# Performance work log

Hardware: AMD Instinct MI355X
Metric: run time of the kernel (lower is better)

Reference implementation:

```python
import jax, jax.numpy as jnp
import numpy as np

E, D, H, W = 512, 64, 64, 64
B, L = 8, 2048
STEPS = 5
OUT_SIGMA_SCALE = 2.0


def setup_inputs() -> dict:
    key = jax.random.key(0)
    ks = jax.random.split(key, 8)
    tokens = jax.random.normal(ks[0], (B, L, E), dtype=jnp.float32)
    # positions on the HxW lattice: col 0 in [0,H), col 1 in [0,W)
    pos = jax.random.uniform(ks[1], (B, L, 2), dtype=jnp.float32)
    positions = pos * jnp.array([H, W], dtype=jnp.float32)
    # learned params (fan-in scaled init, as nn.Linear/Conv2d would give)
    W_to_field = jax.random.normal(ks[2], (D, E), dtype=jnp.float32) / np.sqrt(E)
    W_from_field = jax.random.normal(ks[3], (E, D), dtype=jnp.float32) / np.sqrt(D)
    conv1_w = jax.random.normal(ks[4], (2 * D, D, 3, 3), dtype=jnp.float32) / np.sqrt(D * 9)
    conv1_b = jnp.zeros((2 * D,), dtype=jnp.float32)
    conv2_w = jax.random.normal(ks[5], (D, 2 * D, 1, 1), dtype=jnp.float32) / np.sqrt(2 * D)
    conv2_b = jnp.zeros((D,), dtype=jnp.float32)
    log_sigma = jnp.array(np.log(4.0), dtype=jnp.float32)
    return {
        "tokens": tokens, "positions": positions,
        "W_to_field": W_to_field, "W_from_field": W_from_field,
        "conv1_w": conv1_w, "conv1_b": conv1_b,
        "conv2_w": conv2_w, "conv2_b": conv2_b,
        "log_sigma": log_sigma,
    }


def _conv2d(x, w, b, pad):
    y = jax.lax.conv_general_dilated(
        x, w, window_strides=(1, 1), padding=[(pad, pad), (pad, pad)],
        dimension_numbers=("NCHW", "OIHW", "NCHW"))
    return y + b[None, :, None, None]


def _norm_gauss(dy2, dx2, sigma):
    # (B,L,H,1)+(B,L,1,W) -> (B,L,H,W), normalized over the lattice
    g = jnp.exp(-(dy2 + dx2) / (2.0 * sigma * sigma))
    return g / (jnp.sum(g, axis=(-2, -1), keepdims=True) + 1e-6)


def reference(tokens, positions, W_to_field, W_from_field,
              conv1_w, conv1_b, conv2_w, conv2_b, log_sigma):
    sigma_in = jax.nn.softplus(log_sigma) + 1e-6
    sigma_out = sigma_in * OUT_SIGMA_SCALE

    proj = jnp.einsum("ble,de->bld", tokens, W_to_field)  # (B,L,D)

    grid_y = jnp.arange(H, dtype=jnp.float32)  # (H,)
    grid_x = jnp.arange(W, dtype=jnp.float32)  # (W,)
    dy2 = (grid_y[None, None, :, None] - positions[..., 0][..., None, None]) ** 2  # (B,L,H,1)
    dx2 = (grid_x[None, None, None, :] - positions[..., 1][..., None, None]) ** 2  # (B,L,1,W)

    weights_in = _norm_gauss(dy2, dx2, sigma_in)   # (B,L,H,W)
    field = jnp.einsum("blc,blhw->bchw", proj, weights_in)  # (B,D,H,W)

    for _ in range(STEPS):
        h = jax.nn.relu(_conv2d(field, conv1_w, conv1_b, pad=1))
        field = field + _conv2d(h, conv2_w, conv2_b, pad=0)

    weights_out = _norm_gauss(dy2, dx2, sigma_out)  # (B,L,H,W)
    sampled = jnp.einsum("bchw,blhw->blc", field, weights_out)  # (B,L,D)

    tokens_out = jnp.einsum("bld,ed->ble", sampled, W_from_field)  # (B,L,E)
    return tokens_out
```

## Files before the change

### kernel.cpp

```cpp
#include <hip/hip_runtime.h>
#include <cmath>
#include <cstddef>

#define BB 8
#define LL 2048
#define EE 512
#define DD 64
#define HH 64
#define HW 4096

typedef __attribute__((ext_vector_type(8))) short short8;
typedef __attribute__((ext_vector_type(4))) short short4v;
typedef __attribute__((ext_vector_type(4))) float f32x4;

__device__ __forceinline__ int swz(int row, int k, int ldk) {
    int g = (k >> 3) ^ (row & ((ldk >> 3) - 1));
    return row * ldk + (g << 3) + (k & 7);
}

__device__ __forceinline__ unsigned short f2bf(float f) {
    unsigned u = __builtin_bit_cast(unsigned, f);
    return (unsigned short)((u + 0x7FFFu + ((u >> 16) & 1u)) >> 16);
}
__device__ __forceinline__ short4v cvt4(float4 v) {
    short4v r;
    r[0] = (short)f2bf(v.x); r[1] = (short)f2bf(v.y);
    r[2] = (short)f2bf(v.z); r[3] = (short)f2bf(v.w);
    return r;
}
#define MFMA16(acc, a, b) acc = __builtin_amdgcn_mfma_f32_16x16x32_bf16(a, b, acc, 0, 0, 0)

__global__ __launch_bounds__(256) void k_reorder(const float* __restrict__ w1,
        const float* __restrict__ w2,
        short* __restrict__ w1b, short* __restrict__ w2b) {
    int i = blockIdx.x * 256 + threadIdx.x;
    if (i < 73728) {
        int c = i & 63, o = (i >> 6) & 127, tap = i >> 13;
        w1b[i] = (short)f2bf(w1[(size_t)o * 576 + c * 9 + tap]);
    }
    if (i < 8192) w2b[i] = (short)f2bf(w2[i]);
}

__global__ __launch_bounds__(256) void k_gauss(const float* __restrict__ pos,
        const float* __restrict__ lsig,
        float* __restrict__ gyiT, float* __restrict__ gxiT,
        float* __restrict__ gyoT, float* __restrict__ gxo) {
    __shared__ float red[4][4][64];
    __shared__ float tile[64 * 65];
    int t = threadIdx.x;
    int ll = t & 63, q = t >> 6;
    int b = blockIdx.y, lt = blockIdx.x;
    int bl = b * LL + lt * 64 + ll;
    float py = pos[(size_t)bl * 2 + 0];
    float px = pos[(size_t)bl * 2 + 1];
    float ls = lsig[0];
    float si = log1pf(expf(ls)) + 1e-6f;
    float so = si * 2.0f;
    float ai = 0.5f / (si * si), ao = 0.5f / (so * so);
    float vyi[16], vxi[16], vyo[16], vxo[16];
    float pyi = 0.f, pxi = 0.f, pyo = 0.f, pxo = 0.f;
    #pragma unroll
    for (int j = 0; j < 16; j++) {
        float g = (float)(q * 16 + j);
        float dy = g - py, dx = g - px;
        float dy2 = dy * dy, dx2 = dx * dx;
        vyi[j] = expf(-dy2 * ai); pyi += vyi[j];
        vxi[j] = expf(-dx2 * ai); pxi += vxi[j];
        vyo[j] = expf(-dy2 * ao); pyo += vyo[j];
        vxo[j] = expf(-dx2 * ao); pxo += vxo[j];
    }
    red[0][q][ll] = pyi; red[1][q][ll] = pxi;
    red[2][q][ll] = pyo; red[3][q][ll] = pxo;
    __syncthreads();
    float syi = red[0][0][ll] + red[0][1][ll] + red[0][2][ll] + red[0][3][ll];
    float sxi = red[1][0][ll] + red[1][1][ll] + red[1][2][ll] + red[1][3][ll];
    float syo = red[2][0][ll] + red[2][1][ll] + red[2][2][ll] + red[2][3][ll];
    float sxo = red[3][0][ll] + red[3][1][ll] + red[3][2][ll] + red[3][3][ll];
    float inv_i = 1.0f / (syi * sxi + 1e-6f);
    float inv_o = 1.0f / (syo * sxo + 1e-6f);
    size_t base = (size_t)b * 64 * LL + lt * 64 + ll;
    #pragma unroll
    for (int j = 0; j < 16; j++) {
        size_t off = base + (size_t)(q * 16 + j) * LL;
        gyiT[off] = vyi[j] * inv_i;
        gxiT[off] = vxi[j];
        gyoT[off] = vyo[j] * inv_o;
        tile[(q * 16 + j) * 65 + ll] = vxo[j];
    }
    __syncthreads();
    #pragma unroll
    for (int j = 0; j < 16; j++) {
        int i = t + 256 * j;
        int lo = i >> 6, wo = i & 63;
        gxo[((size_t)b * LL + lt * 64 + lo) * 64 + wo] = tile[wo * 65 + lo];
    }
}

__global__ __launch_bounds__(256) void k_proj(const float* __restrict__ tokens,
        const float* __restrict__ wtf, float* __restrict__ projT) {
    __shared__ __align__(16) short At[4096], Bt[4096];
    int t = threadIdx.x, lane = t & 63, wid = t >> 6;
    int blk = blockIdx.x;
    int b = blk >> 5;
    int l0b = (blk & 31) * 64;
    size_t tokbase = ((size_t)b * LL + l0b) * EE;
    f32x4 z = {0.f, 0.f, 0.f, 0.f};
    f32x4 acc[4] = {z, z, z, z};
    float4 pa[4], pb[4];
    #pragma unroll
    for (int j = 0; j < 4; j++) {
        int idx = t + 256 * j;
        int row = idx >> 4, kq = (idx & 15) << 2;
        pa[j] = *(const float4*)&wtf[(size_t)row * EE + kq];
        pb[j] = *(const float4*)&tokens[tokbase + (size_t)row * EE + kq];
    }
    for (int c = 0; c < 8; c++) {
        __syncthreads();
        #pragma unroll
        for (int j = 0; j < 4; j++) {
            int idx = t + 256 * j;
            int row = idx >> 4, kq = (idx & 15) << 2;
            *(short4v*)&At[swz(row, kq, 64)] = cvt4(pa[j]);
            *(short4v*)&Bt[swz(row, kq, 64)] = cvt4(pb[j]);
        }
        __syncthreads();
        if (c < 7) {
            int e0 = (c + 1) * 64;
            #pragma unroll
            for (int j = 0; j < 4; j++) {
                int idx = t + 256 * j;
                int row = idx >> 4, kq = (idx & 15) << 2;
                pa[j] = *(const float4*)&wtf[(size_t)row * EE + e0 + kq];
                pb[j] = *(const float4*)&tokens[tokbase + (size_t)row * EE + e0 + kq];
            }
        }
        int mrow = wid * 16 + (lane & 15);
        #pragma unroll
        for (int ks = 0; ks < 2; ks++) {
            int k0 = ks * 32 + (lane >> 4) * 8;
            short8 a = *(short8*)&At[swz(mrow, k0, 64)];
            #pragma unroll
            for (int n = 0; n < 4; n++) {
                short8 bb = *(short8*)&Bt[swz(n * 16 + (lane & 15), k0, 64)];
                MFMA16(acc[n], a, bb);
            }
        }
    }
    #pragma unroll
    for (int n = 0; n < 4; n++)
        #pragma unroll
        for (int r = 0; r < 4; r++) {
            int d = wid * 16 + ((lane >> 4) << 2) + r;
            int l = l0b + n * 16 + (lane & 15);
            projT[((size_t)b * 64 + d) * LL + l] = acc[n][r];
        }
}

__global__ __launch_bounds__(256) void k_scatter(const float* __restrict__ projT,
        const float* __restrict__ gyiT, const float* __restrict__ gxiT,
        float* __restrict__ fieldT) {
    __shared__ __align__(16) char smem[24576];
    short* At0 = (short*)smem;
    short* At1 = At0 + 4096;
    short* Bt  = At1 + 4096;
    float* Cf  = (float*)smem;
    int t = threadIdx.x, lane = t & 63, wid = t >> 6;
    int hp = blockIdx.x, b = blockIdx.y;
    int h0 = hp * 2;
    f32x4 z = {0.f, 0.f, 0.f, 0.f};
    f32x4 acc0[4] = {z, z, z, z}, acc1[4] = {z, z, z, z};
    const float* gy0 = gyiT + ((size_t)b * 64 + h0) * LL;
    const float* gy1 = gyiT + ((size_t)b * 64 + h0 + 1) * LL;
    float4 pp[4], pg[4], py0[4], py1[4];
    #pragma unroll
    for (int j = 0; j < 4; j++) {
        int idx = t + 256 * j;
        int row = idx >> 4, kq = (idx & 15) << 2;
        pp[j]  = *(const float4*)&projT[((size_t)b * 64 + row) * LL + kq];
        pg[j]  = *(const float4*)&gxiT[((size_t)b * 64 + row) * LL + kq];
        py0[j] = *(const float4*)&gy0[kq];
        py1[j] = *(const float4*)&gy1[kq];
    }
    for (int c = 0; c < 32; c++) {
        __syncthreads();
        #pragma unroll
        for (int j = 0; j < 4; j++) {
            int idx = t + 256 * j;
            int row = idx >> 4, kq = (idx & 15) << 2;
            float4 a0 = {pp[j].x * py0[j].x, pp[j].y * py0[j].y,
                         pp[j].z * py0[j].z, pp[j].w * py0[j].w};
            float4 a1 = {pp[j].x * py1[j].x, pp[j].y * py1[j].y,
                         pp[j].z * py1[j].z, pp[j].w * py1[j].w};
            *(short4v*)&At0[swz(row, kq, 64)] = cvt4(a0);
            *(short4v*)&At1[swz(row, kq, 64)] = cvt4(a1);
            *(short4v*)&Bt[swz(row, kq, 64)]  = cvt4(pg[j]);
        }
        __syncthreads();
        if (c < 31) {
            int l0 = (c + 1) * 64;
            #pragma unroll
            for (int j = 0; j < 4; j++) {
                int idx = t + 256 * j;
                int row = idx >> 4, kq = (idx & 15) << 2;
                pp[j]  = *(const float4*)&projT[((size_t)b * 64 + row) * LL + l0 + kq];
                pg[j]  = *(const float4*)&gxiT[((size_t)b * 64 + row) * LL + l0 + kq];
                py0[j] = *(const float4*)&gy0[l0 + kq];
                py1[j] = *(const float4*)&gy1[l0 + kq];
            }
        }
        int mrow = wid * 16 + (lane & 15);
        #pragma unroll
        for (int ks = 0; ks < 2; ks++) {
            int k0 = ks * 32 + (lane >> 4) * 8;
            short8 a0 = *(short8*)&At0[swz(mrow, k0, 64)];
            short8 a1 = *(short8*)&At1[swz(mrow, k0, 64)];
            #pragma unroll
            for (int n = 0; n < 4; n++) {
                short8 bb = *(short8*)&Bt[swz(n * 16 + (lane & 15), k0, 64)];
                MFMA16(acc0[n], a0, bb);
                MFMA16(acc1[n], a1, bb);
            }
        }
    }
    #pragma unroll
    for (int p = 0; p < 2; p++) {
        __syncthreads();
        #pragma unroll
        for (int n = 0; n < 4; n++)
            #pragma unroll
            for (int r = 0; r < 4; r++) {
                int w = n * 16 + (lane & 15);
                int cc = wid * 16 + ((lane >> 4) << 2) + r;
                Cf[w * 68 + cc] = (p == 0) ? acc0[n][r] : acc1[n][r];
            }
        __syncthreads();
        #pragma unroll
        for (int j = 0; j < 4; j++) {
            int i = t + 256 * j;
            int wo = i >> 4, cq = (i & 15) << 2;
            *(float4*)&fieldT[(((size_t)b * 64 + h0 + p) * 64 + wo) * 64 + cq] =
                *(float4*)&Cf[wo * 68 + cq];
        }
    }
}

__global__ __launch_bounds__(256) void k_conv(const float* __restrict__ fin,
        float* __restrict__ fout,
        const short* __restrict__ w1b, const float* __restrict__ b1,
        const short* __restrict__ w2b, const float* __restrict__ b2,
        float* __restrict__ fnchw, int final_step) {
    __shared__ __align__(16) char smem[61952];
    short* halo = (short*)smem;
    short* w1t  = (short*)(smem + 12800);
    short* ht   = (short*)(smem + 29184);
    short* w2s  = (short*)(smem + 45568);
    float* Cf   = (float*)smem;
    int t = threadIdx.x, lane = t & 63, wid = t >> 6;
    int tile = blockIdx.x, b = blockIdx.y;
    int y0 = (tile >> 3) << 3, x0 = (tile & 7) << 3;
    const float* fb = fin + (size_t)b * 64 * HW;

    for (int i = t; i < 1600; i += 256) {
        int pix = i >> 4, cq = (i & 15) << 2;
        int pr = pix / 10, pc = pix - pr * 10;
        int gy = y0 + pr - 1, gx = x0 + pc - 1;
        float4 v = {0.f, 0.f, 0.f, 0.f};
        if ((unsigned)gy < 64u && (unsigned)gx < 64u)
            v = *(const float4*)&fb[((size_t)gy * 64 + gx) * 64 + cq];
        *(short4v*)&halo[swz(pix, cq, 64)] = cvt4(v);
    }
    for (int i = t; i < 1024; i += 256) {
        int d = i >> 4, g = i & 15;
        short8 v = *(const short8*)&w2b[(size_t)d * 128 + g * 8];
        *(short8*)&w2s[swz(d, g * 8, 128)] = v;
    }
    f32x4 accH[8];
    #pragma unroll
    for (int n = 0; n < 8; n++) {
        float bv = b1[n * 16 + (lane & 15)];
        f32x4 v = {bv, bv, bv, bv};
        accH[n] = v;
    }
    short8 w1pf[4];
    #pragma unroll
    for (int j = 0; j < 4; j++) {
        int i = t + 256 * j;
        int o = i >> 3, g = i & 7;
        w1pf[j] = *(const short8*)&w1b[((size_t)o) * 64 + g * 8];
    }
    int mpix = wid * 16 + (lane & 15);
    int ppy = mpix >> 3, ppx = mpix & 7;

    #pragma unroll
    for (int tap = 0; tap < 9; tap++) {
        int ky = tap / 3, kx = tap - ky * 3;
        __syncthreads();
        #pragma unroll
        for (int j = 0; j < 4; j++) {
            int i = t + 256 * j;
            int o = i >> 3, g = i & 7;
            *(short8*)&w1t[swz(o, g * 8, 64)] = w1pf[j];
        }
        __syncthreads();
        if (tap < 8) {
            #pragma unroll
            for (int j = 0; j < 4; j++) {
                int i = t + 256 * j;
                int o = i >> 3, g = i & 7;
                w1pf[j] = *(const short8*)&w1b[((size_t)(tap + 1) * 128 + o) * 64 + g * 8];
            }
        }
        int hpix = (ppy + ky) * 10 + (ppx + kx);
        #pragma unroll
        for (int ks = 0; ks < 2; ks++) {
            int k0 = ks * 32 + (lane >> 4) * 8;
            short8 a = *(short8*)&halo[swz(hpix, k0, 64)];
            #pragma unroll
            for (int n = 0; n < 8; n++) {
                short8 bb = *(short8*)&w1t[swz(n * 16 + (lane & 15), k0, 64)];
                MFMA16(accH[n], a, bb);
            }
        }
    }
    #pragma unroll
    for (int n = 0; n < 8; n++)
        #pragma unroll
        for (int r = 0; r < 4; r++) {
            int m = wid * 16 + ((lane >> 4) << 2) + r;
            int o = n * 16 + (lane & 15);
            ht[swz(m, o, 128)] = (short)f2bf(fmaxf(accH[n][r], 0.f));
        }
    __syncthreads();
    f32x4 acc2[4];
    #pragma unroll
    for (int n = 0; n < 4; n++) {
        float bv = b2[n * 16 + (lane & 15)];
        f32x4 v = {bv, bv, bv, bv};
        acc2[n] = v;
    }
    #pragma unroll
    for (int ks = 0; ks < 4; ks++) {
        int k0 = ks * 32 + (lane >> 4) * 8;
        short8 a = *(short8*)&ht[swz(mpix, k0, 128)];
        #pragma unroll
        for (int n = 0; n < 4; n++) {
            short8 bb = *(short8*)&w2s[swz(n * 16 + (lane & 15), k0, 128)];
            MFMA16(acc2[n], a, bb);
        }
    }
    float* fo = fout + (size_t)b * 64 * HW;
    #pragma unroll
    for (int n = 0; n < 4; n++)
        #pragma unroll
        for (int r = 0; r < 4; r++) {
            int m = wid * 16 + ((lane >> 4) << 2) + r;
            int py = m >> 3, px = m & 7;
            int d = n * 16 + (lane & 15);
            size_t addr = (((size_t)(y0 + py)) * 64 + x0 + px) * 64 + d;
            float val = acc2[n][r] + fb[addr];
            fo[addr] = val;
            if (final_step) Cf[d * 68 + m] = val;
        }
    if (final_step) {
        __syncthreads();
        #pragma unroll
        for (int j = 0; j < 4; j++) {
            int i = t + 256 * j;
            int d = i >> 4, pq = (i & 15) << 2;
            int py = pq >> 3, px = pq & 7;
            *(float4*)&fnchw[(((size_t)b * 64 + d) * 64 + y0 + py) * 64 + x0 + px] =
                *(float4*)&Cf[d * 68 + pq];
        }
    }
}

__global__ __launch_bounds__(256) void k_gather(const float* __restrict__ fnchw,
        const float* __restrict__ gyoT, const float* __restrict__ gxo,
        float* __restrict__ sampz) {
    __shared__ __align__(16) short At[4096], Bt[4096];
    int t = threadIdx.x, lane = t & 63, wid = t >> 6;
    int lt = blockIdx.x, b = blockIdx.y, zz = blockIdx.z;
    int l0 = lt * 64;
    f32x4 z4 = {0.f, 0.f, 0.f, 0.f};
    f32x4 acc[4] = {z4, z4, z4, z4};
    float4 ga[4], fbq[4];
    float gys[4];
    #pragma unroll
    for (int j = 0; j < 4; j++) {
        int idx = t + 256 * j;
        int row = idx >> 4, wq = (idx & 15) << 2;
        ga[j] = *(const float4*)&gxo[((size_t)b * LL + l0 + row) * 64 + wq];
    }
    {
        int h = zz * 32;
        #pragma unroll
        for (int j = 0; j < 4; j++) {
            int idx = t + 256 * j;
            int row = idx >> 4, wq = (idx & 15) << 2;
            gys[j] = gyoT[((size_t)b * 64 + h) * LL + l0 + row];
            fbq[j] = *(const float4*)&fnchw[(((size_t)b * 64 + row) * 64 + h) * 64 + wq];
        }
    }
    for (int c = 0; c < 32; c++) {
        __syncthreads();
        #pragma unroll
        for (int j = 0; j < 4; j++) {
            int idx = t + 256 * j;
            int row = idx >> 4, wq = (idx & 15) << 2;
            float4 a = {ga[j].x * gys[j], ga[j].y * gys[j],
                        ga[j].z * gys[j], ga[j].w * gys[j]};
            *(short4v*)&At[swz(row, wq, 64)] = cvt4(a);
            *(short4v*)&Bt[swz(row, wq, 64)] = cvt4(fbq[j]);
        }
        __syncthreads();
        if (c < 31) {
            int h = zz * 32 + c + 1;
            #pragma unroll
            for (int j = 0; j < 4; j++) {
                int idx = t + 256 * j;
                int row = idx >> 4, wq = (idx & 15) << 2;
                gys[j] = gyoT[((size_t)b * 64 + h) * LL + l0 + row];
                fbq[j] = *(const float4*)&fnchw[(((size_t)b * 64 + row) * 64 + h) * 64 + wq];
            }
        }
        int mrow = wid * 16 + (lane & 15);
        #pragma unroll
        for (int ks = 0; ks < 2; ks++) {
            int k0 = ks * 32 + (lane >> 4) * 8;
            short8 a = *(short8*)&At[swz(mrow, k0, 64)];
            #pragma unroll
            for (int n = 0; n < 4; n++) {
                short8 bb = *(short8*)&Bt[swz(n * 16 + (lane & 15), k0, 64)];
                MFMA16(acc[n], a, bb);
            }
        }
    }
    #pragma unroll
    for (int n = 0; n < 4; n++)
        #pragma unroll
        for (int r = 0; r < 4; r++) {
            int lr = wid * 16 + ((lane >> 4) << 2) + r;
            int cc = n * 16 + (lane & 15);
            sampz[(((size_t)zz * BB + b) * LL + l0 + lr) * 64 + cc] = acc[n][r];
        }
}

__global__ __launch_bounds__(256) void k_out(const float* __restrict__ s0,
        const float* __restrict__ s1, const float* __restrict__ wff,
        float* __restrict__ out) {
    __shared__ __align__(16) short At[4096], Bt[4096];
    int t = threadIdx.x, lane = t & 63, wid = t >> 6;
    int mt = blockIdx.x, e0 = blockIdx.y * 64;
    #pragma unroll
    for (int j = 0; j < 4; j++) {
        int idx = t + 256 * j;
        int row = idx >> 4, kq = (idx & 15) << 2;
        float4 v0 = *(const float4*)&s0[((size_t)mt * 64 + row) * 64 + kq];
        float4 v1 = *(const float4*)&s1[((size_t)mt * 64 + row) * 64 + kq];
        float4 vs = {v0.x + v1.x, v0.y + v1.y, v0.z + v1.z, v0.w + v1.w};
        *(short4v*)&At[swz(row, kq, 64)] = cvt4(vs);
        float4 wv = *(const float4*)&wff[(size_t)(e0 + row) * 64 + kq];
        *(short4v*)&Bt[swz(row, kq, 64)] = cvt4(wv);
    }
    __syncthreads();
    f32x4 z = {0.f, 0.f, 0.f, 0.f};
    f32x4 acc[4] = {z, z, z, z};
    int mrow = wid * 16 + (lane & 15);
    #pragma unroll
    for (int ks = 0; ks < 2; ks++) {
        int k0 = ks * 32 + (lane >> 4) * 8;
        short8 a = *(short8*)&At[swz(mrow, k0, 64)];
        #pragma unroll
        for (int n = 0; n < 4; n++) {
            short8 bb = *(short8*)&Bt[swz(n * 16 + (lane & 15), k0, 64)];
            MFMA16(acc[n], a, bb);
        }
    }
    #pragma unroll
    for (int n = 0; n < 4; n++)
        #pragma unroll
        for (int r = 0; r < 4; r++) {
            int lr = wid * 16 + ((lane >> 4) << 2) + r;
            int ec = e0 + n * 16 + (lane & 15);
            out[((size_t)mt * 64 + lr) * EE + ec] = acc[n][r];
        }
}

extern "C" void kernel_launch(void* const* d_in, const int* in_sizes, int n_in,
                              void* d_out, int out_size, void* d_ws, size_t ws_size,
                              hipStream_t stream) {
    const float* tokens = (const float*)d_in[0];
    const float* pos    = (const float*)d_in[1];
    const float* wtf    = (const float*)d_in[2];
    const float* wff    = (const float*)d_in[3];
    const float* w1     = (const float*)d_in[4];
    const float* b1     = (const float*)d_in[5];
    const float* w2     = (const float*)d_in[6];
    const float* b2     = (const float*)d_in[7];
    const float* lsig   = (const float*)d_in[8];
    float* out = (float*)d_out;

    const size_t M1 = 1048576;
    float* ws    = (float*)d_ws;
    float* gyiT  = ws;
    float* gxiT  = ws + 1 * M1;
    float* projT = ws + 2 * M1;
    float* gyoT  = ws + 3 * M1;
    float* gxo   = ws + 4 * M1;
    float* fA    = ws + 5 * M1;
    float* fB    = ws + 7 * M1;
    short* w1b   = (short*)(ws + 9 * M1);
    short* w2b   = w1b + 73728;
    float* fnchw = ws;
    float* samp0 = ws + 7 * M1;
    float* samp1 = ws + 8 * M1;

    hipLaunchKernelGGL(k_reorder, dim3(288), dim3(256), 0, stream, w1, w2, w1b, w2b);
    hipLaunchKernelGGL(k_gauss, dim3(32, 8), dim3(256), 0, stream,
                       pos, lsig, gyiT, gxiT, gyoT, gxo);
    hipLaunchKernelGGL(k_proj, dim3(256), dim3(256), 0, stream, tokens, wtf, projT);
    hipLaunchKernelGGL(k_scatter, dim3(32, 8), dim3(256), 0, stream,
                       projT, gyiT, gxiT, fA);
    const float* ci = fA;
    float* co = fB;
    for (int s = 0; s < 5; s++) {
        hipLaunchKernelGGL(k_conv, dim3(64, 8), dim3(256), 0, stream,
                           ci, co, w1b, b1, w2b, b2, fnchw, (s == 4) ? 1 : 0);
        float* tmp = co; co = (float*)ci; ci = tmp;
    }
    hipLaunchKernelGGL(k_gather, dim3(32, 8, 2), dim3(256), 0, stream,
                       fnchw, gyoT, gxo, samp0);
    hipLaunchKernelGGL(k_out, dim3(256, 8), dim3(256), 0, stream,
                       samp0, samp1, wff, out);
}
```

Before: 260.3 us.

## Store intermediates in bf16, split-K scatter/gather, double-buffer conv weights

Gaussian weights, projection and the final field are now stored as bf16 instead of fp32, which halves intermediate memory traffic. The scatter is split four ways along L with a new reduction kernel, and the gather is split four ways along H, both to raise parallelism. The conv kernel double-buffers its per-tap weight tiles in shared memory to drop one barrier per tap, and skips writing the field on the final step. It also restructures the scatter factorization (gx*gy product moved to the B operand), at the cost of extra partial buffers, more LDS, and lower-precision storage.

Result: faster. 244.1 us (-6.2%).

```diff
diff --git a/kernel.cpp b/kernel.cpp
--- a/kernel.cpp
+++ b/kernel.cpp
@@ -5,8 +5,6 @@
 #define BB 8
 #define LL 2048
 #define EE 512
-#define DD 64
-#define HH 64
 #define HW 4096
 
 typedef __attribute__((ext_vector_type(8))) short short8;
@@ -17,10 +15,12 @@
     int g = (k >> 3) ^ (row & ((ldk >> 3) - 1));
     return row * ldk + (g << 3) + (k & 7);
 }
-
 __device__ __forceinline__ unsigned short f2bf(float f) {
     unsigned u = __builtin_bit_cast(unsigned, f);
     return (unsigned short)((u + 0x7FFFu + ((u >> 16) & 1u)) >> 16);
+}
+__device__ __forceinline__ float bf2f(short s) {
+    return __builtin_bit_cast(float, (unsigned)((unsigned short)s) << 16);
 }
 __device__ __forceinline__ short4v cvt4(float4 v) {
     short4v r;
@@ -43,8 +43,8 @@
 
 __global__ __launch_bounds__(256) void k_gauss(const float* __restrict__ pos,
         const float* __restrict__ lsig,
-        float* __restrict__ gyiT, float* __restrict__ gxiT,
-        float* __restrict__ gyoT, float* __restrict__ gxo) {
+        short* __restrict__ gyiT, short* __restrict__ gxiT,
+        short* __restrict__ gyoT, short* __restrict__ gxo) {
     __shared__ float red[4][4][64];
     __shared__ float tile[64 * 65];
     int t = threadIdx.x;
@@ -82,9 +82,9 @@
     #pragma unroll
     for (int j = 0; j < 16; j++) {
         size_t off = base + (size_t)(q * 16 + j) * LL;
-        gyiT[off] = vyi[j] * inv_i;
-        gxiT[off] = vxi[j];
-        gyoT[off] = vyo[j] * inv_o;
+        gyiT[off] = (short)f2bf(vyi[j] * inv_i);
+        gxiT[off] = (short)f2bf(vxi[j]);
+        gyoT[off] = (short)f2bf(vyo[j] * inv_o);
         tile[(q * 16 + j) * 65 + ll] = vxo[j];
     }
     __syncthreads();
@@ -92,12 +92,12 @@
     for (int j = 0; j < 16; j++) {
         int i = t + 256 * j;
         int lo = i >> 6, wo = i & 63;
-        gxo[((size_t)b * LL + lt * 64 + lo) * 64 + wo] = tile[wo * 65 + lo];
+        gxo[((size_t)b * LL + lt * 64 + lo) * 64 + wo] = (short)f2bf(tile[wo * 65 + lo]);
     }
 }
 
 __global__ __launch_bounds__(256) void k_proj(const float* __restrict__ tokens,
-        const float* __restrict__ wtf, float* __restrict__ projT) {
+        const float* __restrict__ wtf, short* __restrict__ projT) {
     __shared__ __align__(16) short At[4096], Bt[4096];
     int t = threadIdx.x, lane = t & 63, wid = t >> 6;
     int blk = blockIdx.x;
@@ -152,76 +152,79 @@
         for (int r = 0; r < 4; r++) {
             int d = wid * 16 + ((lane >> 4) << 2) + r;
             int l = l0b + n * 16 + (lane & 15);
-            projT[((size_t)b * 64 + d) * LL + l] = acc[n][r];
-        }
-}
-
-__global__ __launch_bounds__(256) void k_scatter(const float* __restrict__ projT,
-        const float* __restrict__ gyiT, const float* __restrict__ gxiT,
-        float* __restrict__ fieldT) {
+            projT[((size_t)b * 64 + d) * LL + l] = (short)f2bf(acc[n][r]);
+        }
+}
+
+__global__ __launch_bounds__(256) void k_scatter(const short* __restrict__ projT,
+        const short* __restrict__ gyiT, const short* __restrict__ gxiT,
+        float* __restrict__ fz) {
     __shared__ __align__(16) char smem[24576];
-    short* At0 = (short*)smem;
-    short* At1 = At0 + 4096;
-    short* Bt  = At1 + 4096;
-    float* Cf  = (float*)smem;
+    short* At = (short*)smem;
+    short* B0 = At + 4096;
+    short* B1 = B0 + 4096;
+    float* Cf = (float*)smem;
     int t = threadIdx.x, lane = t & 63, wid = t >> 6;
-    int hp = blockIdx.x, b = blockIdx.y;
+    int hp = blockIdx.x, b = blockIdx.y, kz = blockIdx.z;
     int h0 = hp * 2;
+    const short* pj  = projT + (size_t)b * 64 * LL + kz * 512;
+    const short* gx  = gxiT + (size_t)b * 64 * LL + kz * 512;
+    const short* gy0 = gyiT + ((size_t)b * 64 + h0) * LL + kz * 512;
+    const short* gy1 = gy0 + LL;
     f32x4 z = {0.f, 0.f, 0.f, 0.f};
     f32x4 acc0[4] = {z, z, z, z}, acc1[4] = {z, z, z, z};
-    const float* gy0 = gyiT + ((size_t)b * 64 + h0) * LL;
-    const float* gy1 = gyiT + ((size_t)b * 64 + h0 + 1) * LL;
-    float4 pp[4], pg[4], py0[4], py1[4];
-    #pragma unroll
-    for (int j = 0; j < 4; j++) {
-        int idx = t + 256 * j;
-        int row = idx >> 4, kq = (idx & 15) << 2;
-        pp[j]  = *(const float4*)&projT[((size_t)b * 64 + row) * LL + kq];
-        pg[j]  = *(const float4*)&gxiT[((size_t)b * 64 + row) * LL + kq];
-        py0[j] = *(const float4*)&gy0[kq];
-        py1[j] = *(const float4*)&gy1[kq];
-    }
-    for (int c = 0; c < 32; c++) {
-        __syncthreads();
-        #pragma unroll
-        for (int j = 0; j < 4; j++) {
-            int idx = t + 256 * j;
-            int row = idx >> 4, kq = (idx & 15) << 2;
-            float4 a0 = {pp[j].x * py0[j].x, pp[j].y * py0[j].y,
-                         pp[j].z * py0[j].z, pp[j].w * py0[j].w};
-            float4 a1 = {pp[j].x * py1[j].x, pp[j].y * py1[j].y,
-                         pp[j].z * py1[j].z, pp[j].w * py1[j].w};
-            *(short4v*)&At0[swz(row, kq, 64)] = cvt4(a0);
-            *(short4v*)&At1[swz(row, kq, 64)] = cvt4(a1);
-            *(short4v*)&Bt[swz(row, kq, 64)]  = cvt4(pg[j]);
-        }
-        __syncthreads();
-        if (c < 31) {
+    short8 pA[2], pX[2], pY0[2], pY1[2];
+    #pragma unroll
+    for (int j = 0; j < 2; j++) {
+        int i = t + 256 * j; int row = i >> 3, g = i & 7;
+        pA[j]  = *(const short8*)&pj[(size_t)row * LL + g * 8];
+        pX[j]  = *(const short8*)&gx[(size_t)row * LL + g * 8];
+        pY0[j] = *(const short8*)&gy0[g * 8];
+        pY1[j] = *(const short8*)&gy1[g * 8];
+    }
+    for (int c = 0; c < 8; c++) {
+        __syncthreads();
+        #pragma unroll
+        for (int j = 0; j < 2; j++) {
+            int i = t + 256 * j; int row = i >> 3, g = i & 7;
+            short8 b0v, b1v;
+            #pragma unroll
+            for (int e = 0; e < 8; e++) {
+                float gxv = bf2f(pX[j][e]);
+                b0v[e] = (short)f2bf(gxv * bf2f(pY0[j][e]));
+                b1v[e] = (short)f2bf(gxv * bf2f(pY1[j][e]));
+            }
+            *(short8*)&At[swz(row, g * 8, 64)] = pA[j];
+            *(short8*)&B0[swz(row, g * 8, 64)] = b0v;
+            *(short8*)&B1[swz(row, g * 8, 64)] = b1v;
+        }
+        __syncthreads();
+        if (c < 7) {
             int l0 = (c + 1) * 64;
             #pragma unroll
-            for (int j = 0; j < 4; j++) {
-                int idx = t + 256 * j;
-                int row = idx >> 4, kq = (idx & 15) << 2;
-                pp[j]  = *(const float4*)&projT[((size_t)b * 64 + row) * LL + l0 + kq];
-                pg[j]  = *(const float4*)&gxiT[((size_t)b * 64 + row) * LL + l0 + kq];
-                py0[j] = *(const float4*)&gy0[l0 + kq];
-                py1[j] = *(const float4*)&gy1[l0 + kq];
+            for (int j = 0; j < 2; j++) {
+                int i = t + 256 * j; int row = i >> 3, g = i & 7;
+                pA[j]  = *(const short8*)&pj[(size_t)row * LL + l0 + g * 8];
+                pX[j]  = *(const short8*)&gx[(size_t)row * LL + l0 + g * 8];
+                pY0[j] = *(const short8*)&gy0[l0 + g * 8];
+                pY1[j] = *(const short8*)&gy1[l0 + g * 8];
             }
         }
         int mrow = wid * 16 + (lane & 15);
         #pragma unroll
         for (int ks = 0; ks < 2; ks++) {
             int k0 = ks * 32 + (lane >> 4) * 8;
-            short8 a0 = *(short8*)&At0[swz(mrow, k0, 64)];
-            short8 a1 = *(short8*)&At1[swz(mrow, k0, 64)];
+            short8 a = *(short8*)&At[swz(mrow, k0, 64)];
             #pragma unroll
             for (int n = 0; n < 4; n++) {
-                short8 bb = *(short8*)&Bt[swz(n * 16 + (lane & 15), k0, 64)];
-                MFMA16(acc0[n], a0, bb);
-                MFMA16(acc1[n], a1, bb);
-            }
-        }
-    }
+                short8 b0f = *(short8*)&B0[swz(n * 16 + (lane & 15), k0, 64)];
+                short8 b1f = *(short8*)&B1[swz(n * 16 + (lane & 15), k0, 64)];
+                MFMA16(acc0[n], a, b0f);
+                MFMA16(acc1[n], a, b1f);
+            }
+        }
+    }
+    float* dst = fz + (size_t)kz * 2097152;
     #pragma unroll
     for (int p = 0; p < 2; p++) {
         __syncthreads();
@@ -238,22 +241,35 @@
         for (int j = 0; j < 4; j++) {
             int i = t + 256 * j;
             int wo = i >> 4, cq = (i & 15) << 2;
-            *(float4*)&fieldT[(((size_t)b * 64 + h0 + p) * 64 + wo) * 64 + cq] =
+            *(float4*)&dst[(((size_t)b * 64 + h0 + p) * 64 + wo) * 64 + cq] =
                 *(float4*)&Cf[wo * 68 + cq];
         }
     }
+}
+
+__global__ __launch_bounds__(256) void k_redfield(const float* __restrict__ fz,
+        float* __restrict__ fA) {
+    const size_t FP = 2097152;
+    size_t i = ((size_t)blockIdx.x * 256 + threadIdx.x) * 4;
+    float4 a = *(const float4*)&fz[i];
+    float4 b = *(const float4*)&fz[i + FP];
+    float4 c = *(const float4*)&fz[i + 2 * FP];
+    float4 d = *(const float4*)&fz[i + 3 * FP];
+    float4 r = {a.x + b.x + c.x + d.x, a.y + b.y + c.y + d.y,
+                a.z + b.z + c.z + d.z, a.w + b.w + c.w + d.w};
+    *(float4*)&fA[i] = r;
 }
 
 __global__ __launch_bounds__(256) void k_conv(const float* __restrict__ fin,
         float* __restrict__ fout,
         const short* __restrict__ w1b, const float* __restrict__ b1,
         const short* __restrict__ w2b, const float* __restrict__ b2,
-        float* __restrict__ fnchw, int final_step) {
-    __shared__ __align__(16) char smem[61952];
+        short* __restrict__ fnchw, int final_step) {
+    __shared__ __align__(16) char smem[78336];
     short* halo = (short*)smem;
     short* w1t  = (short*)(smem + 12800);
-    short* ht   = (short*)(smem + 29184);
-    short* w2s  = (short*)(smem + 45568);
+    short* ht   = (short*)(smem + 45568);
+    short* w2s  = (short*)(smem + 61952);
     float* Cf   = (float*)smem;
     int t = threadIdx.x, lane = t & 63, wid = t >> 6;
     int tile = blockIdx.x, b = blockIdx.y;
@@ -274,6 +290,11 @@
         short8 v = *(const short8*)&w2b[(size_t)d * 128 + g * 8];
         *(short8*)&w2s[swz(d, g * 8, 128)] = v;
     }
+    #pragma unroll
+    for (int j = 0; j < 4; j++) {
+        int i = t + 256 * j; int o = i >> 3, g = i & 7;
+        *(short8*)&w1t[swz(o, g * 8, 64)] = *(const short8*)&w1b[(size_t)o * 64 + g * 8];
+    }
     f32x4 accH[8];
     #pragma unroll
     for (int n = 0; n < 8; n++) {
@@ -281,35 +302,35 @@
         f32x4 v = {bv, bv, bv, bv};
         accH[n] = v;
     }
+    __syncthreads();
     short8 w1pf[4];
     #pragma unroll
     for (int j = 0; j < 4; j++) {
-        int i = t + 256 * j;
-        int o = i >> 3, g = i & 7;
-        w1pf[j] = *(const short8*)&w1b[((size_t)o) * 64 + g * 8];
+        int i = t + 256 * j; int o = i >> 3, g = i & 7;
+        w1pf[j] = *(const short8*)&w1b[((size_t)128 + o) * 64 + g * 8];
     }
     int mpix = wid * 16 + (lane & 15);
     int ppy = mpix >> 3, ppx = mpix & 7;
 
     #pragma unroll
     for (int tap = 0; tap < 9; tap++) {
+        short* buf = w1t + (tap & 1) * 8192;
+        if (tap < 8) {
+            short* nbuf = w1t + ((tap + 1) & 1) * 8192;
+            #pragma unroll
+            for (int j = 0; j < 4; j++) {
+                int i = t + 256 * j; int o = i >> 3, g = i & 7;
+                *(short8*)&nbuf[swz(o, g * 8, 64)] = w1pf[j];
+            }
+            if (tap < 7) {
+                #pragma unroll
+                for (int j = 0; j < 4; j++) {
+                    int i = t + 256 * j; int o = i >> 3, g = i & 7;
+                    w1pf[j] = *(const short8*)&w1b[((size_t)(tap + 2) * 128 + o) * 64 + g * 8];
+                }
+            }
+        }
         int ky = tap / 3, kx = tap - ky * 3;
-        __syncthreads();
-        #pragma unroll
-        for (int j = 0; j < 4; j++) {
-            int i = t + 256 * j;
-            int o = i >> 3, g = i & 7;
-            *(short8*)&w1t[swz(o, g * 8, 64)] = w1pf[j];
-        }
-        __syncthreads();
-        if (tap < 8) {
-            #pragma unroll
-            for (int j = 0; j < 4; j++) {
-                int i = t + 256 * j;
-                int o = i >> 3, g = i & 7;
-                w1pf[j] = *(const short8*)&w1b[((size_t)(tap + 1) * 128 + o) * 64 + g * 8];
-            }
-        }
         int hpix = (ppy + ky) * 10 + (ppx + kx);
         #pragma unroll
         for (int ks = 0; ks < 2; ks++) {
@@ -317,10 +338,11 @@
             short8 a = *(short8*)&halo[swz(hpix, k0, 64)];
             #pragma unroll
             for (int n = 0; n < 8; n++) {
-                short8 bb = *(short8*)&w1t[swz(n * 16 + (lane & 15), k0, 64)];
+                short8 bb = *(short8*)&buf[swz(n * 16 + (lane & 15), k0, 64)];
                 MFMA16(accH[n], a, bb);
             }
         }
+        __syncthreads();
     }
     #pragma unroll
     for (int n = 0; n < 8; n++)
@@ -358,8 +380,8 @@
             int d = n * 16 + (lane & 15);
             size_t addr = (((size_t)(y0 + py)) * 64 + x0 + px) * 64 + d;
             float val = acc2[n][r] + fb[addr];
-            fo[addr] = val;
-            if (final_step) Cf[d * 68 + m] = val;
+            if (!final_step) fo[addr] = val;
+            else Cf[d * 68 + m] = val;
         }
     if (final_step) {
         __syncthreads();
@@ -368,14 +390,15 @@
             int i = t + 256 * j;
             int d = i >> 4, pq = (i & 15) << 2;
             int py = pq >> 3, px = pq & 7;
-            *(float4*)&fnchw[(((size_t)b * 64 + d) * 64 + y0 + py) * 64 + x0 + px] =
-                *(float4*)&Cf[d * 68 + pq];
-        }
-    }
-}
-
-__global__ __launch_bounds__(256) void k_gather(const float* __restrict__ fnchw,
-        const float* __restrict__ gyoT, const float* __restrict__ gxo,
+            float4 v = *(float4*)&Cf[d * 68 + pq];
+            *(short4v*)&fnchw[(((size_t)b * 64 + d) * 64 + y0 + py) * 64 + x0 + px] =
+                cvt4(v);
+        }
+    }
+}
+
+__global__ __launch_bounds__(256) void k_gather(const short* __restrict__ fnchw,
+        const short* __restrict__ gyoT, const short* __restrict__ gxo,
         float* __restrict__ sampz) {
     __shared__ __align__(16) short At[4096], Bt[4096];
     int t = threadIdx.x, lane = t & 63, wid = t >> 6;
@@ -383,44 +406,40 @@
     int l0 = lt * 64;
     f32x4 z4 = {0.f, 0.f, 0.f, 0.f};
     f32x4 acc[4] = {z4, z4, z4, z4};
-    float4 ga[4], fbq[4];
-    float gys[4];
-    #pragma unroll
-    for (int j = 0; j < 4; j++) {
-        int idx = t + 256 * j;
-        int row = idx >> 4, wq = (idx & 15) << 2;
-        ga[j] = *(const float4*)&gxo[((size_t)b * LL + l0 + row) * 64 + wq];
-    }
-    {
-        int h = zz * 32;
-        #pragma unroll
-        for (int j = 0; j < 4; j++) {
-            int idx = t + 256 * j;
-            int row = idx >> 4, wq = (idx & 15) << 2;
-            gys[j] = gyoT[((size_t)b * 64 + h) * LL + l0 + row];
-            fbq[j] = *(const float4*)&fnchw[(((size_t)b * 64 + row) * 64 + h) * 64 + wq];
-        }
-    }
-    for (int c = 0; c < 32; c++) {
-        __syncthreads();
-        #pragma unroll
-        for (int j = 0; j < 4; j++) {
-            int idx = t + 256 * j;
-            int row = idx >> 4, wq = (idx & 15) << 2;
-            float4 a = {ga[j].x * gys[j], ga[j].y * gys[j],
-                        ga[j].z * gys[j], ga[j].w * gys[j]};
-            *(short4v*)&At[swz(row, wq, 64)] = cvt4(a);
-            *(short4v*)&Bt[swz(row, wq, 64)] = cvt4(fbq[j]);
-        }
-        __syncthreads();
-        if (c < 31) {
-            int h = zz * 32 + c + 1;
-            #pragma unroll
-            for (int j = 0; j < 4; j++) {
-                int idx = t + 256 * j;
-                int row = idx >> 4, wq = (idx & 15) << 2;
-                gys[j] = gyoT[((size_t)b * 64 + h) * LL + l0 + row];
-                fbq[j] = *(const float4*)&fnchw[(((size_t)b * 64 + row) * 64 + h) * 64 + wq];
+    short8 pX[2], pF[2];
+    float gyv[2];
+    #pragma unroll
+    for (int j = 0; j < 2; j++) {
+        int i = t + 256 * j; int row = i >> 3, g = i & 7;
+        pX[j] = *(const short8*)&gxo[((size_t)b * LL + l0 + row) * 64 + g * 8];
+    }
+    int h0 = zz * 16;
+    #pragma unroll
+    for (int j = 0; j < 2; j++) {
+        int i = t + 256 * j; int row = i >> 3, g = i & 7;
+        gyv[j] = bf2f(gyoT[((size_t)b * 64 + h0) * LL + l0 + row]);
+        pF[j] = *(const short8*)&fnchw[(((size_t)b * 64 + row) * 64 + h0) * 64 + g * 8];
+    }
+    for (int c = 0; c < 16; c++) {
+        __syncthreads();
+        #pragma unroll
+        for (int j = 0; j < 2; j++) {
+            int i = t + 256 * j; int row = i >> 3, g = i & 7;
+            short8 a;
+            #pragma unroll
+            for (int e = 0; e < 8; e++)
+                a[e] = (short)f2bf(bf2f(pX[j][e]) * gyv[j]);
+            *(short8*)&At[swz(row, g * 8, 64)] = a;
+            *(short8*)&Bt[swz(row, g * 8, 64)] = pF[j];
+        }
+        __syncthreads();
+        if (c < 15) {
+            int h = h0 + c + 1;
+            #pragma unroll
+            for (int j = 0; j < 2; j++) {
+                int i = t + 256 * j; int row = i >> 3, g = i & 7;
+                gyv[j] = bf2f(gyoT[((size_t)b * 64 + h) * LL + l0 + row]);
+                pF[j] = *(const short8*)&fnchw[(((size_t)b * 64 + row) * 64 + h) * 64 + g * 8];
             }
         }
         int mrow = wid * 16 + (lane & 15);
@@ -445,19 +464,23 @@
         }
 }
 
-__global__ __launch_bounds__(256) void k_out(const float* __restrict__ s0,
-        const float* __restrict__ s1, const float* __restrict__ wff,
-        float* __restrict__ out) {
+__global__ __launch_bounds__(256) void k_out(const float* __restrict__ samp,
+        const float* __restrict__ wff, float* __restrict__ out) {
     __shared__ __align__(16) short At[4096], Bt[4096];
+    const size_t SP = 1048576;
     int t = threadIdx.x, lane = t & 63, wid = t >> 6;
     int mt = blockIdx.x, e0 = blockIdx.y * 64;
     #pragma unroll
     for (int j = 0; j < 4; j++) {
         int idx = t + 256 * j;
         int row = idx >> 4, kq = (idx & 15) << 2;
-        float4 v0 = *(const float4*)&s0[((size_t)mt * 64 + row) * 64 + kq];
-        float4 v1 = *(const float4*)&s1[((size_t)mt * 64 + row) * 64 + kq];
-        float4 vs = {v0.x + v1.x, v0.y + v1.y, v0.z + v1.z, v0.w + v1.w};
+        size_t off = ((size_t)mt * 64 + row) * 64 + kq;
+        float4 v0 = *(const float4*)&samp[off];
+        float4 v1 = *(const float4*)&samp[off + SP];
+        float4 v2 = *(const float4*)&samp[off + 2 * SP];
+        float4 v3 = *(const float4*)&samp[off + 3 * SP];
+        float4 vs = {v0.x + v1.x + v2.x + v3.x, v0.y + v1.y + v2.y + v3.y,
+                     v0.z + v1.z + v2.z + v3.z, v0.w + v1.w + v2.w + v3.w};
         *(short4v*)&At[swz(row, kq, 64)] = cvt4(vs);
         float4 wv = *(const float4*)&wff[(size_t)(e0 + row) * 64 + kq];
         *(short4v*)&Bt[swz(row, kq, 64)] = cvt4(wv);
@@ -502,25 +525,27 @@
 
     const size_t M1 = 1048576;
     float* ws    = (float*)d_ws;
-    float* gyiT  = ws;
-    float* gxiT  = ws + 1 * M1;
-    float* projT = ws + 2 * M1;
-    float* gyoT  = ws + 3 * M1;
-    float* gxo   = ws + 4 * M1;
-    float* fA    = ws + 5 * M1;
-    float* fB    = ws + 7 * M1;
-    short* w1b   = (short*)(ws + 9 * M1);
+    short* sbase = (short*)d_ws;
+    short* gyiT  = sbase;
+    short* gxiT  = sbase + 1 * M1;
+    short* gyoT  = sbase + 2 * M1;
+    short* gxo   = sbase + 3 * M1;
+    short* projT = sbase + 4 * M1;
+    float* fz    = ws + 3 * M1;
+    float* fA    = ws + 11 * M1;
+    float* fB    = ws + 13 * M1;
+    short* fnchw = (short*)(ws + 15 * M1);
+    float* samp  = ws + 16 * M1;
+    short* w1b   = (short*)(ws + 20 * M1);
     short* w2b   = w1b + 73728;
-    float* fnchw = ws;
-    float* samp0 = ws + 7 * M1;
-    float* samp1 = ws + 8 * M1;
 
     hipLaunchKernelGGL(k_reorder, dim3(288), dim3(256), 0, stream, w1, w2, w1b, w2b);
     hipLaunchKernelGGL(k_gauss, dim3(32, 8), dim3(256), 0, stream,
                        pos, lsig, gyiT, gxiT, gyoT, gxo);
     hipLaunchKernelGGL(k_proj, dim3(256), dim3(256), 0, stream, tokens, wtf, projT);
-    hipLaunchKernelGGL(k_scatter, dim3(32, 8), dim3(256), 0, stream,
-                       projT, gyiT, gxiT, fA);
+    hipLaunchKernelGGL(k_scatter, dim3(32, 8, 4), dim3(256), 0, stream,
+                       projT, gyiT, gxiT, fz);
+    hipLaunchKernelGGL(k_redfield, dim3(2048), dim3(256), 0, stream, fz, fA);
     const float* ci = fA;
     float* co = fB;
     for (int s = 0; s < 5; s++) {
@@ -528,8 +553,8 @@
                            ci, co, w1b, b1, w2b, b2, fnchw, (s == 4) ? 1 : 0);
         float* tmp = co; co = (float*)ci; ci = tmp;
     }
-    hipLaunchKernelGGL(k_gather, dim3(32, 8, 2), dim3(256), 0, stream,
-                       fnchw, gyoT, gxo, samp0);
+    hipLaunchKernelGGL(k_gather, dim3(32, 8, 4), dim3(256), 0, stream,
+                       fnchw, gyoT, gxo, samp);
     hipLaunchKernelGGL(k_out, dim3(256, 8), dim3(256), 0, stream,
-                       samp0, samp1, wff, out);
-}
+                       samp, wff, out);
+}
```
